# Optimization experiments

Hardware: AMD Instinct MI355X
Metric: run time of the kernel (lower is better)

The kernel has to match this reference:

```python
import jax, jax.numpy as jnp
import numpy as np

N = 50000   # nodes
E = 800000  # edges per timestep
T = 2
IN_C = 128
HID = 128


def gcn_conv(x, src, dst, W, b):
    """PyG GCNConv: add self-loops, symmetric normalization, linear, scatter-add, bias."""
    n = x.shape[0]
    loop = jnp.arange(n, dtype=src.dtype)
    s = jnp.concatenate([src, loop])  # [E+N]
    d = jnp.concatenate([dst, loop])
    h = x @ W                          # [N, H]
    deg = jax.ops.segment_sum(jnp.ones_like(d, dtype=x.dtype), d, num_segments=n)
    dinv = jnp.where(deg > 0, jax.lax.rsqrt(deg), 0.0)
    norm = dinv[s] * dinv[d]           # [E+N]
    msg = h[s] * norm[:, None]         # gather + scale
    out = jax.ops.segment_sum(msg, d, num_segments=n)  # scatter-add
    return out + b


def setup_inputs() -> dict:
    key = jax.random.key(0)
    ks = jax.random.split(key, 6)
    x_seq = jax.random.normal(ks[0], (T, N, IN_C), dtype=jnp.float32)
    edge_indices = jax.random.randint(ks[1], (T, 2, E), 0, N, dtype=jnp.int64)
    W1 = jax.random.normal(ks[2], (IN_C, HID), dtype=jnp.float32) * (1.0 / np.sqrt(IN_C))
    b1 = jnp.zeros((HID,), dtype=jnp.float32)
    W2 = jax.random.normal(ks[3], (HID, HID), dtype=jnp.float32) * (1.0 / np.sqrt(HID))
    b2 = jnp.zeros((HID,), dtype=jnp.float32)
    Wc = jax.random.normal(ks[4], (HID, 1), dtype=jnp.float32) * (1.0 / np.sqrt(HID))
    bc = jnp.zeros((1,), dtype=jnp.float32)
    return {"x_seq": x_seq, "edge_indices": edge_indices, "W1": W1, "b1": b1,
            "W2": W2, "b2": b2, "Wc": Wc, "bc": bc}


def reference(x_seq, edge_indices, W1, b1, W2, b2, Wc, bc):
    outputs = []
    for t in range(T):  # small fixed timestep loop, as in original
        x_t = x_seq[t]
        src = edge_indices[t, 0]
        dst = edge_indices[t, 1]
        h = jax.nn.relu(gcn_conv(x_t, src, dst, W1, b1))
        # dropout is inference-identity (eval mode)
        h = gcn_conv(h, src, dst, W2, b2)
        outputs.append(h)
    final = outputs[-1]
    importance_out = (final @ Wc + bc).squeeze(-1)  # [N]
    return (importance_out, *outputs)
```

## Files before the change

kernel.cpp:

```cpp
#include <hip/hip_runtime.h>
#include <hip/hip_bf16.h>

typedef unsigned int u32;
typedef unsigned short u16;
typedef unsigned long long u64;
typedef __bf16 bf16x8 __attribute__((ext_vector_type(8)));
typedef short short8 __attribute__((ext_vector_type(8)));
typedef float floatx4 __attribute__((ext_vector_type(4)));

__device__ inline float b2f(u16 b) { return __uint_as_float((u32)b << 16); }
__device__ inline float lo2f(u32 p) { return __uint_as_float(p << 16); }
__device__ inline float hi2f(u32 p) { return __uint_as_float(p & 0xffff0000u); }
__device__ inline u16 f2bs(float f) {
    __hip_bfloat16 h = __float2bfloat16(f);
    return *reinterpret_cast<u16*>(&h);
}
__device__ inline float ldext(const void* p, int fl, int i) {
    return fl ? ((const float*)p)[i] : b2f(((const u16*)p)[i]);
}

__global__ __launch_bounds__(64) void detect_kernel(const int* __restrict__ eb,
                                                    const u32* __restrict__ xw,
                                                    int* __restrict__ flags,
                                                    int S, int n) {
    __shared__ int sh[64 * 3];
    int lane = threadIdx.x & 63;
    int zc = 0, explo = 0;
#pragma unroll
    for (int r = 0; r < 4; ++r) {
        int i = 64 * r + lane;
        zc += (eb[2 * i + 1] == 0) ? 1 : 0;
        u32 w = xw[i];
        int e = (int)((w >> 7) & 0xFF);
        explo += (e >= 96 && e <= 140) ? 1 : 0;
    }
    sh[lane] = zc;
    sh[64 + lane] = explo;
    __syncthreads();
    int fl = 0;
    {
        int z = 0;
        for (int j = 0; j < 64; ++j) z += sh[j];
        fl = (z > 200) ? 1 : 0;
    }
    int vc = 0;
#pragma unroll
    for (int r = 0; r < 4; ++r) {
        int li = S / 2 + 64 * r + lane;
        int v = fl ? eb[2 * li] : eb[li];
        vc += ((unsigned)v < (unsigned)n) ? 1 : 0;
    }
    sh[128 + lane] = vc;
    __syncthreads();
    if (lane == 0) {
        int vtot = 0, etot = 0;
        for (int j = 0; j < 64; ++j) vtot += sh[128 + j];
        for (int j = 0; j < 64; ++j) etot += sh[64 + j];
        flags[0] = fl;
        flags[1] = (etot >= 192) ? 0 : 1;
        flags[2] = (vtot >= 240) ? (S / 4) : (S / 8);
    }
}

__device__ inline int load_edge(const int* eb, int fl, int idx) {
    return eb[fl ? (idx << 1) : idx];
}

#define PCHUNK 4096
__global__ __launch_bounds__(256) void part_kernel(const int* __restrict__ eb,
                                                   const int* __restrict__ flags,
                                                   int* __restrict__ bkcnt,
                                                   u64* __restrict__ pairs,
                                                   int n, int shift, int capP) {
    __shared__ int cnt[512];
    __shared__ int gbase[512];
    const int E = flags[2];
    const int fl = flags[0];
    const int nbuk = (2 * n + (1 << shift) - 1) >> shift;
    const int tid = threadIdx.x;
    for (int i = tid; i < nbuk; i += 256) cnt[i] = 0;
    __syncthreads();
    const int e0 = blockIdx.x * PCHUNK;
    int sv[16], gv[16], rk[16];
#pragma unroll
    for (int j = 0; j < 16; ++j) {
        int e = e0 + j * 256 + tid;
        int s = 0, g = -1;
        if (e < 2 * E) {
            int t = (e >= E) ? 1 : 0;
            int le = e - t * E;
            s = load_edge(eb, fl, t * 2 * E + le);
            unsigned du = (unsigned)load_edge(eb, fl, t * 2 * E + E + le);
            if (du < (unsigned)n) g = t * n + (int)du;
        }
        sv[j] = s;
        gv[j] = g;
        rk[j] = (g >= 0) ? atomicAdd(&cnt[g >> shift], 1) : 0;
    }
    __syncthreads();
    for (int b = tid; b < nbuk; b += 256) {
        int c = cnt[b];
        gbase[b] = c ? atomicAdd(&bkcnt[b], c) : 0;
    }
    __syncthreads();
#pragma unroll
    for (int j = 0; j < 16; ++j) {
        if (gv[j] >= 0) {
            int b = gv[j] >> shift;
            int idx = gbase[b] + rk[j];
            if (idx < capP)
                pairs[(size_t)b * capP + idx] =
                    ((u64)(u32)gv[j] << 32) | (u32)sv[j];
        }
    }
}

__global__ __launch_bounds__(256) void scan_bk(const int* __restrict__ bkcnt,
                                               int* __restrict__ bkbase,
                                               int nbuk, int capP) {
    __shared__ int tmp[256];
    int t = threadIdx.x;
    int carry = 0;
    for (int c0 = 0; c0 < nbuk; c0 += 256) {
        int d = 0;
        if (c0 + t < nbuk) {
            d = bkcnt[c0 + t];
            if (d > capP) d = capP;
        }
        int val = d;
        tmp[t] = val;
        __syncthreads();
        for (int o = 1; o < 256; o <<= 1) {
            int add = (t >= o) ? tmp[t - o] : 0;
            __syncthreads();
            val += add;
            tmp[t] = val;
            __syncthreads();
        }
        if (c0 + t < nbuk) bkbase[c0 + t] = val - d + carry;
        int tot = tmp[255];
        __syncthreads();
        carry += tot;
    }
}

__global__ __launch_bounds__(256) void scat_kernel(const u64* __restrict__ pairs,
                                                   const int* __restrict__ bkcnt,
                                                   const int* __restrict__ bkbase,
                                                   int* __restrict__ deg,
                                                   int* __restrict__ off,
                                                   float* __restrict__ dinv,
                                                   int* __restrict__ ssrc,
                                                   int n2, int shift, int capP) {
    __shared__ int hist[1024];
    __shared__ int lscan[256];
    const int b = blockIdx.x;
    const int d0 = b << shift;
    if (d0 >= n2) return;
    int nn = (1 << shift);
    if (d0 + nn > n2) nn = n2 - d0;
    const int tid = threadIdx.x;
    for (int j = tid; j < nn; j += 256) hist[j] = 0;
    __syncthreads();
    int cnt = bkcnt[b];
    if (cnt > capP) cnt = capP;
    const u64* pb = pairs + (size_t)b * capP;
    for (int i = tid; i < cnt; i += 256) {
        unsigned dl = (unsigned)(int)(pb[i] >> 32) - (unsigned)d0;
        if (dl < (unsigned)nn) atomicAdd(&hist[dl], 1);
    }
    __syncthreads();
    int base4 = tid * 4;
    int s0 = 0, s1 = 0, s2 = 0, s3 = 0;
    if (base4 < nn) {
        s0 = hist[base4];
        s1 = (base4 + 1 < nn) ? hist[base4 + 1] : 0;
        s2 = (base4 + 2 < nn) ? hist[base4 + 2] : 0;
        s3 = (base4 + 3 < nn) ? hist[base4 + 3] : 0;
    }
    int tsum = s0 + s1 + s2 + s3;
    lscan[tid] = tsum;
    __syncthreads();
    int val = tsum;
    for (int o = 1; o < 256; o <<= 1) {
        int add = (tid >= o) ? lscan[tid - o] : 0;
        __syncthreads();
        val += add;
        lscan[tid] = val;
        __syncthreads();
    }
    int texcl = val - tsum;
    const int gb = bkbase[b];
    if (base4 < nn) {
        int g = d0 + base4;
        int o0 = gb + texcl;
        deg[g] = s0; off[g] = o0; dinv[g] = rsqrtf((float)(s0 + 1));
        hist[base4] = o0;
        if (base4 + 1 < nn) {
            int o1 = o0 + s0;
            deg[g + 1] = s1; off[g + 1] = o1; dinv[g + 1] = rsqrtf((float)(s1 + 1));
            hist[base4 + 1] = o1;
        }
        if (base4 + 2 < nn) {
            int o2 = o0 + s0 + s1;
            deg[g + 2] = s2; off[g + 2] = o2; dinv[g + 2] = rsqrtf((float)(s2 + 1));
            hist[base4 + 2] = o2;
        }
        if (base4 + 3 < nn) {
            int o3 = o0 + s0 + s1 + s2;
            deg[g + 3] = s3; off[g + 3] = o3; dinv[g + 3] = rsqrtf((float)(s3 + 1));
            hist[base4 + 3] = o3;
        }
    }
    __syncthreads();
    const int limit = gb + cnt;
    for (int i = tid; i < cnt; i += 256) {
        u64 p = pb[i];
        unsigned dl = (unsigned)(int)(p >> 32) - (unsigned)d0;
        if (dl < (unsigned)nn) {
            int pos = atomicAdd(&hist[dl], 1);
            if (pos < limit) ssrc[pos] = (int)(u32)p;
        }
    }
}

__global__ __launch_bounds__(256) void prep_w(const void* __restrict__ W1,
                                              const void* __restrict__ W2,
                                              const int* __restrict__ flags,
                                              u16* __restrict__ W1t,
                                              u16* __restrict__ W2t) {
    int tid = blockIdx.x * 256 + threadIdx.x;
    if (tid < 2 * 128 * 128) {
        int which = tid >> 14;
        int r = tid & 16383;
        const void* W = which ? W2 : W1;
        u16* Wt = which ? W2t : W1t;
        int c = r >> 7, k = r & 127;
        Wt[c * 128 + k] = f2bs(ldext(W, flags[1], k * 128 + c));
    }
}

__global__ __launch_bounds__(256) void gemm_mfma(const void* __restrict__ Xv,
                                                 size_t xoff, int x_ext,
                                                 const u16* __restrict__ Wt,
                                                 const int* __restrict__ flags,
                                                 const float* __restrict__ dinv,
                                                 u16* __restrict__ hs, int n) {
    __shared__ u16 Ws[128 * 136];
    {
        u32* wsu = (u32*)Ws;
        const u32* wtu = (const u32*)Wt;
        for (int i = threadIdx.x; i < 128 * 64; i += 256) {
            int c = i >> 6, kk = i & 63;
            wsu[c * 68 + kk] = wtu[i];
        }
    }
    __syncthreads();

    const int wave = threadIdx.x >> 6;
    const int lane = threadIdx.x & 63;
    const int m = lane & 15;
    const int quad = lane >> 4;
    const int node0 = blockIdx.x * 64 + wave * 16;
    if (node0 >= n) return;

    const int xf32 = x_ext ? flags[1] : 0;
    int va = node0 + m;
    if (va > n - 1) va = n - 1;

    floatx4 acc[8];
#pragma unroll
    for (int t = 0; t < 8; ++t) acc[t] = (floatx4){0.f, 0.f, 0.f, 0.f};

#pragma unroll
    for (int ks = 0; ks < 4; ++ks) {
        bf16x8 a;
        if (xf32) {
            const float* Xf = (const float*)Xv + xoff + (size_t)va * 128 + ks * 32 + quad * 8;
            float4 x0 = *(const float4*)Xf;
            float4 x1 = *(const float4*)(Xf + 4);
            short8 as;
            as[0] = (short)f2bs(x0.x); as[1] = (short)f2bs(x0.y);
            as[2] = (short)f2bs(x0.z); as[3] = (short)f2bs(x0.w);
            as[4] = (short)f2bs(x1.x); as[5] = (short)f2bs(x1.y);
            as[6] = (short)f2bs(x1.z); as[7] = (short)f2bs(x1.w);
            a = __builtin_bit_cast(bf16x8, as);
        } else {
            const u16* Xb = (const u16*)Xv + xoff + (size_t)va * 128 + ks * 32 + quad * 8;
            a = *(const bf16x8*)Xb;
        }
#pragma unroll
        for (int t = 0; t < 8; ++t) {
            const bf16x8 b = *(const bf16x8*)(Ws + (16 * t + m) * 136 + ks * 32 + quad * 8);
            acc[t] = __builtin_amdgcn_mfma_f32_16x16x32_bf16(a, b, acc[t], 0, 0, 0);
        }
    }

#pragma unroll
    for (int r = 0; r < 4; ++r) {
        int v = node0 + quad * 4 + r;
        if (v < n) {
            float dv = dinv[v];
#pragma unroll
            for (int t = 0; t < 8; ++t)
                hs[(size_t)v * 128 + 16 * t + m] = f2bs(acc[t][r] * dv);
        }
    }
}

__global__ __launch_bounds__(256) void gather_kernel(const u16* __restrict__ hs,
                                                     const int* __restrict__ off,
                                                     const int* __restrict__ deg,
                                                     const int* __restrict__ ssrc,
                                                     const float* __restrict__ dinv,
                                                     const void* __restrict__ bias,
                                                     const int* __restrict__ flags,
                                                     float* __restrict__ outf,
                                                     u16* __restrict__ outb,
                                                     const void* __restrict__ Wc,
                                                     const void* __restrict__ bc,
                                                     float* __restrict__ imp,
                                                     int n, int relu) {
    int w = (blockIdx.x * 256 + threadIdx.x) >> 6;
    int lane = threadIdx.x & 63;
    if (w >= n) return;

    const u32* hsu = (const u32*)hs;
    u32 p = hsu[(size_t)w * 64 + lane];
    float ax = lo2f(p), ay = hi2f(p);
    int i = __builtin_amdgcn_readfirstlane(off[w]);
    int end = i + __builtin_amdgcn_readfirstlane(deg[w]);
    unsigned nm1 = (unsigned)(n - 1);

    float bx = 0.f, by = 0.f, cx = 0.f, cy = 0.f, dx = 0.f, dy = 0.f;
    for (; i + 8 <= end; i += 8) {
        unsigned s0 = (unsigned)ssrc[i];     if (s0 > nm1) s0 = 0;
        unsigned s1 = (unsigned)ssrc[i + 1]; if (s1 > nm1) s1 = 0;
        unsigned s2 = (unsigned)ssrc[i + 2]; if (s2 > nm1) s2 = 0;
        unsigned s3 = (unsigned)ssrc[i + 3]; if (s3 > nm1) s3 = 0;
        unsigned s4 = (unsigned)ssrc[i + 4]; if (s4 > nm1) s4 = 0;
        unsigned s5 = (unsigned)ssrc[i + 5]; if (s5 > nm1) s5 = 0;
        unsigned s6 = (unsigned)ssrc[i + 6]; if (s6 > nm1) s6 = 0;
        unsigned s7 = (unsigned)ssrc[i + 7]; if (s7 > nm1) s7 = 0;
        u32 v0 = hsu[(size_t)s0 * 64 + lane];
        u32 v1 = hsu[(size_t)s1 * 64 + lane];
        u32 v2 = hsu[(size_t)s2 * 64 + lane];
        u32 v3 = hsu[(size_t)s3 * 64 + lane];
        u32 v4 = hsu[(size_t)s4 * 64 + lane];
        u32 v5 = hsu[(size_t)s5 * 64 + lane];
        u32 v6 = hsu[(size_t)s6 * 64 + lane];
        u32 v7 = hsu[(size_t)s7 * 64 + lane];
        ax += lo2f(v0); ay += hi2f(v0);
        bx += lo2f(v1); by += hi2f(v1);
        cx += lo2f(v2); cy += hi2f(v2);
        dx += lo2f(v3); dy += hi2f(v3);
        ax += lo2f(v4); ay += hi2f(v4);
        bx += lo2f(v5); by += hi2f(v5);
        cx += lo2f(v6); cy += hi2f(v6);
        dx += lo2f(v7); dy += hi2f(v7);
    }
    for (; i + 4 <= end; i += 4) {
        unsigned s0 = (unsigned)ssrc[i];     if (s0 > nm1) s0 = 0;
        unsigned s1 = (unsigned)ssrc[i + 1]; if (s1 > nm1) s1 = 0;
        unsigned s2 = (unsigned)ssrc[i + 2]; if (s2 > nm1) s2 = 0;
        unsigned s3 = (unsigned)ssrc[i + 3]; if (s3 > nm1) s3 = 0;
        u32 v0 = hsu[(size_t)s0 * 64 + lane];
        u32 v1 = hsu[(size_t)s1 * 64 + lane];
        u32 v2 = hsu[(size_t)s2 * 64 + lane];
        u32 v3 = hsu[(size_t)s3 * 64 + lane];
        ax += lo2f(v0); ay += hi2f(v0);
        bx += lo2f(v1); by += hi2f(v1);
        cx += lo2f(v2); cy += hi2f(v2);
        dx += lo2f(v3); dy += hi2f(v3);
    }
    for (; i < end; ++i) {
        unsigned s = (unsigned)ssrc[i];
        if (s > nm1) s = 0;
        u32 v = hsu[(size_t)s * 64 + lane];
        ax += lo2f(v);
        ay += hi2f(v);
    }
    ax += bx + cx + dx;
    ay += by + cy + dy;

    int ffl = flags[1];
    float dv = dinv[w];
    float o0 = dv * ax + ldext(bias, ffl, 2 * lane);
    float o1 = dv * ay + ldext(bias, ffl, 2 * lane + 1);
    if (relu) {
        o0 = fmaxf(o0, 0.f);
        o1 = fmaxf(o1, 0.f);
    }
    if (outf) ((float2*)outf)[(size_t)w * 64 + lane] = make_float2(o0, o1);
    else ((u32*)outb)[(size_t)w * 64 + lane] = (u32)f2bs(o0) | ((u32)f2bs(o1) << 16);

    if (imp) {
        float cb = o0 * ldext(Wc, ffl, 2 * lane) + o1 * ldext(Wc, ffl, 2 * lane + 1);
        cb += __shfl_xor(cb, 32);
        cb += __shfl_xor(cb, 16);
        cb += __shfl_xor(cb, 8);
        cb += __shfl_xor(cb, 4);
        cb += __shfl_xor(cb, 2);
        cb += __shfl_xor(cb, 1);
        if (lane == 0) imp[w] = cb + ldext(bc, ffl, 0);
    }
}

extern "C" void kernel_launch(void* const* d_in, const int* in_sizes, int n_in,
                              void* d_out, int out_size, void* d_ws, size_t ws_size,
                              hipStream_t stream) {
    const int T = 2, C = 128;
    const int N = in_sizes[0] / (T * C);
    const int S = in_sizes[1];
    const int Emax = S / 4;
    const int N2 = 2 * N;

    const void* x_seq = d_in[0];
    const int* edges = (const int*)d_in[1];
    const void* W1 = d_in[2];
    const void* b1 = d_in[3];
    const void* W2 = d_in[4];
    const void* b2 = d_in[5];
    const void* Wc = d_in[6];
    const void* bc = d_in[7];

    float* out = (float*)d_out;
    float* R0 = out + N;
    float* R1 = out + N + (size_t)N * C;

    char* p = (char*)d_ws;
    auto alloc = [&](size_t bytes) {
        char* r = p;
        p += (bytes + 255) & ~(size_t)255;
        return r;
    };
    int* flags = (int*)alloc(256);
    int* deg = (int*)alloc((size_t)N2 * 4);
    int* off = (int*)alloc((size_t)N2 * 4);
    float* dinv = (float*)alloc((size_t)N2 * 4);
    int* bkcnt = (int*)alloc(512 * 4);
    int* bkbase = (int*)alloc(512 * 4);
    int* ssrc = (int*)alloc((size_t)2 * Emax * 4);
    u16* W1t = (u16*)alloc(128 * 128 * 2);
    u16* W2t = (u16*)alloc(128 * 128 * 2);
    u16* hsb = (u16*)alloc((size_t)N * C * 2);
    u16* hmb = (u16*)alloc((size_t)N * C * 2);
    u64* pairs = (u64*)hsb;

    int shift = 8;
    while ((((N2 + (1 << shift) - 1) >> shift) > 512) && shift < 10) ++shift;
    const int NBUK = (N2 + (1 << shift) - 1) >> shift;
    const size_t aliasBytes = (size_t)2 * N * C * 2;
    int capP = (int)(aliasBytes / (8 * (size_t)NBUK));

    const int gP = (2 * Emax + PCHUNK - 1) / PCHUNK;
    const int gN4 = (N + 3) / 4;
    const int gG = (N + 63) / 64;
    const int gW = (2 * 128 * 128 + 255) / 256;

    detect_kernel<<<1, 64, 0, stream>>>(edges, (const u32*)x_seq, flags, S, N);
    prep_w<<<gW, 256, 0, stream>>>(W1, W2, flags, W1t, W2t);

    hipMemsetAsync(bkcnt, 0, 512 * 4, stream);
    part_kernel<<<gP, 256, 0, stream>>>(edges, flags, bkcnt, pairs, N, shift, capP);
    scan_bk<<<1, 256, 0, stream>>>(bkcnt, bkbase, NBUK, capP);
    scat_kernel<<<NBUK, 256, 0, stream>>>(pairs, bkcnt, bkbase, deg, off, dinv,
                                          ssrc, N2, shift, capP);

    for (int t = 0; t < T; ++t) {
        float* Rt = (t == 0) ? R0 : R1;
        const int* off_t = off + (size_t)t * N;
        const int* deg_t = deg + (size_t)t * N;
        const float* dinv_t = dinv + (size_t)t * N;

        gemm_mfma<<<gG, 256, 0, stream>>>(x_seq, (size_t)t * N * C, 1, W1t, flags,
                                          dinv_t, hsb, N);
        gather_kernel<<<gN4, 256, 0, stream>>>(hsb, off_t, deg_t, ssrc, dinv_t, b1,
                                               flags, (float*)nullptr, hmb,
                                               nullptr, nullptr, (float*)nullptr,
                                               N, 1);

        gemm_mfma<<<gG, 256, 0, stream>>>(hmb, 0, 0, W2t, flags, dinv_t, hsb, N);
        gather_kernel<<<gN4, 256, 0, stream>>>(hsb, off_t, deg_t, ssrc, dinv_t, b2,
                                               flags, Rt, (u16*)nullptr,
                                               Wc, bc, (t == 1) ? out : (float*)nullptr,
                                               N, 0);
    }
}
```

Baseline: 327.8 us.

## Batch both timesteps into single GEMM/gather launches and drop bucket scan

Measured after the change: 293.2 us. 10.5% less time.

```diff
diff --git a/kernel.cpp b/kernel.cpp
--- a/kernel.cpp
+++ b/kernel.cpp
@@ -81,19 +81,19 @@
     for (int i = tid; i < nbuk; i += 256) cnt[i] = 0;
     __syncthreads();
     const int e0 = blockIdx.x * PCHUNK;
-    int sv[16], gv[16], rk[16];
+    u32 sv[16]; int gv[16], rk[16];
 #pragma unroll
     for (int j = 0; j < 16; ++j) {
         int e = e0 + j * 256 + tid;
-        int s = 0, g = -1;
+        u32 gs = 0; int g = -1;
         if (e < 2 * E) {
             int t = (e >= E) ? 1 : 0;
             int le = e - t * E;
-            s = load_edge(eb, fl, t * 2 * E + le);
+            gs = (u32)(t * n) + (u32)load_edge(eb, fl, t * 2 * E + le);
             unsigned du = (unsigned)load_edge(eb, fl, t * 2 * E + E + le);
             if (du < (unsigned)n) g = t * n + (int)du;
         }
-        sv[j] = s;
+        sv[j] = gs;
         gv[j] = g;
         rk[j] = (g >= 0) ? atomicAdd(&cnt[g >> shift], 1) : 0;
     }
@@ -110,43 +110,13 @@
             int idx = gbase[b] + rk[j];
             if (idx < capP)
                 pairs[(size_t)b * capP + idx] =
-                    ((u64)(u32)gv[j] << 32) | (u32)sv[j];
-        }
-    }
-}
-
-__global__ __launch_bounds__(256) void scan_bk(const int* __restrict__ bkcnt,
-                                               int* __restrict__ bkbase,
-                                               int nbuk, int capP) {
-    __shared__ int tmp[256];
-    int t = threadIdx.x;
-    int carry = 0;
-    for (int c0 = 0; c0 < nbuk; c0 += 256) {
-        int d = 0;
-        if (c0 + t < nbuk) {
-            d = bkcnt[c0 + t];
-            if (d > capP) d = capP;
-        }
-        int val = d;
-        tmp[t] = val;
-        __syncthreads();
-        for (int o = 1; o < 256; o <<= 1) {
-            int add = (t >= o) ? tmp[t - o] : 0;
-            __syncthreads();
-            val += add;
-            tmp[t] = val;
-            __syncthreads();
-        }
-        if (c0 + t < nbuk) bkbase[c0 + t] = val - d + carry;
-        int tot = tmp[255];
-        __syncthreads();
-        carry += tot;
+                    ((u64)(u32)gv[j] << 32) | sv[j];
+        }
     }
 }
 
 __global__ __launch_bounds__(256) void scat_kernel(const u64* __restrict__ pairs,
                                                    const int* __restrict__ bkcnt,
-                                                   const int* __restrict__ bkbase,
                                                    int* __restrict__ deg,
                                                    int* __restrict__ off,
                                                    float* __restrict__ dinv,
@@ -164,7 +134,8 @@
     __syncthreads();
     int cnt = bkcnt[b];
     if (cnt > capP) cnt = capP;
-    const u64* pb = pairs + (size_t)b * capP;
+    const int gb = b * capP;
+    const u64* pb = pairs + (size_t)gb;
     for (int i = tid; i < cnt; i += 256) {
         unsigned dl = (unsigned)(int)(pb[i] >> 32) - (unsigned)d0;
         if (dl < (unsigned)nn) atomicAdd(&hist[dl], 1);
@@ -190,7 +161,6 @@
         __syncthreads();
     }
     int texcl = val - tsum;
-    const int gb = bkbase[b];
     if (base4 < nn) {
         int g = d0 + base4;
         int o0 = gb + texcl;
@@ -241,7 +211,7 @@
 }
 
 __global__ __launch_bounds__(256) void gemm_mfma(const void* __restrict__ Xv,
-                                                 size_t xoff, int x_ext,
+                                                 int x_ext,
                                                  const u16* __restrict__ Wt,
                                                  const int* __restrict__ flags,
                                                  const float* __restrict__ dinv,
@@ -276,7 +246,7 @@
     for (int ks = 0; ks < 4; ++ks) {
         bf16x8 a;
         if (xf32) {
-            const float* Xf = (const float*)Xv + xoff + (size_t)va * 128 + ks * 32 + quad * 8;
+            const float* Xf = (const float*)Xv + (size_t)va * 128 + ks * 32 + quad * 8;
             float4 x0 = *(const float4*)Xf;
             float4 x1 = *(const float4*)(Xf + 4);
             short8 as;
@@ -286,7 +256,7 @@
             as[6] = (short)f2bs(x1.z); as[7] = (short)f2bs(x1.w);
             a = __builtin_bit_cast(bf16x8, as);
         } else {
-            const u16* Xb = (const u16*)Xv + xoff + (size_t)va * 128 + ks * 32 + quad * 8;
+            const u16* Xb = (const u16*)Xv + (size_t)va * 128 + ks * 32 + quad * 8;
             a = *(const bf16x8*)Xb;
         }
 #pragma unroll
@@ -320,17 +290,17 @@
                                                      const void* __restrict__ Wc,
                                                      const void* __restrict__ bc,
                                                      float* __restrict__ imp,
-                                                     int n, int relu) {
+                                                     int n2, int half, int relu) {
     int w = (blockIdx.x * 256 + threadIdx.x) >> 6;
     int lane = threadIdx.x & 63;
-    if (w >= n) return;
+    if (w >= n2) return;
 
     const u32* hsu = (const u32*)hs;
     u32 p = hsu[(size_t)w * 64 + lane];
     float ax = lo2f(p), ay = hi2f(p);
     int i = __builtin_amdgcn_readfirstlane(off[w]);
     int end = i + __builtin_amdgcn_readfirstlane(deg[w]);
-    unsigned nm1 = (unsigned)(n - 1);
+    unsigned nm1 = (unsigned)(n2 - 1);
 
     float bx = 0.f, by = 0.f, cx = 0.f, cy = 0.f, dx = 0.f, dy = 0.f;
     for (; i + 8 <= end; i += 8) {
@@ -394,7 +364,7 @@
     if (outf) ((float2*)outf)[(size_t)w * 64 + lane] = make_float2(o0, o1);
     else ((u32*)outb)[(size_t)w * 64 + lane] = (u32)f2bs(o0) | ((u32)f2bs(o1) << 16);
 
-    if (imp) {
+    if (imp && w >= half) {
         float cb = o0 * ldext(Wc, ffl, 2 * lane) + o1 * ldext(Wc, ffl, 2 * lane + 1);
         cb += __shfl_xor(cb, 32);
         cb += __shfl_xor(cb, 16);
@@ -402,7 +372,7 @@
         cb += __shfl_xor(cb, 4);
         cb += __shfl_xor(cb, 2);
         cb += __shfl_xor(cb, 1);
-        if (lane == 0) imp[w] = cb + ldext(bc, ffl, 0);
+        if (lane == 0) imp[w - half] = cb + ldext(bc, ffl, 0);
     }
 }
 
@@ -414,6 +384,7 @@
     const int S = in_sizes[1];
     const int Emax = S / 4;
     const int N2 = 2 * N;
+    (void)Emax;
 
     const void* x_seq = d_in[0];
     const int* edges = (const int*)d_in[1];
@@ -425,8 +396,7 @@
     const void* bc = d_in[7];
 
     float* out = (float*)d_out;
-    float* R0 = out + N;
-    float* R1 = out + N + (size_t)N * C;
+    float* R = out + N;
 
     char* p = (char*)d_ws;
     auto alloc = [&](size_t bytes) {
@@ -439,23 +409,23 @@
     int* off = (int*)alloc((size_t)N2 * 4);
     float* dinv = (float*)alloc((size_t)N2 * 4);
     int* bkcnt = (int*)alloc(512 * 4);
-    int* bkbase = (int*)alloc(512 * 4);
-    int* ssrc = (int*)alloc((size_t)2 * Emax * 4);
-    u16* W1t = (u16*)alloc(128 * 128 * 2);
-    u16* W2t = (u16*)alloc(128 * 128 * 2);
-    u16* hsb = (u16*)alloc((size_t)N * C * 2);
-    u16* hmb = (u16*)alloc((size_t)N * C * 2);
-    u64* pairs = (u64*)hsb;
 
     int shift = 8;
     while ((((N2 + (1 << shift) - 1) >> shift) > 512) && shift < 10) ++shift;
     const int NBUK = (N2 + (1 << shift) - 1) >> shift;
-    const size_t aliasBytes = (size_t)2 * N * C * 2;
-    int capP = (int)(aliasBytes / (8 * (size_t)NBUK));
+    const size_t aliasBytes = (size_t)2 * N2 * C * 2;
+    const int capP = (int)(aliasBytes / (8 * (size_t)NBUK));
+
+    int* ssrc = (int*)alloc((size_t)NBUK * capP * 4);
+    u16* W1t = (u16*)alloc(128 * 128 * 2);
+    u16* W2t = (u16*)alloc(128 * 128 * 2);
+    u16* hsb = (u16*)alloc((size_t)N2 * C * 2);
+    u16* hmb = (u16*)alloc((size_t)N2 * C * 2);
+    u64* pairs = (u64*)hsb;
 
     const int gP = (2 * Emax + PCHUNK - 1) / PCHUNK;
-    const int gN4 = (N + 3) / 4;
-    const int gG = (N + 63) / 64;
+    const int gN2 = (N2 + 3) / 4;
+    const int gG2 = (N2 + 63) / 64;
     const int gW = (2 * 128 * 128 + 255) / 256;
 
     detect_kernel<<<1, 64, 0, stream>>>(edges, (const u32*)x_seq, flags, S, N);
@@ -463,27 +433,18 @@
 
     hipMemsetAsync(bkcnt, 0, 512 * 4, stream);
     part_kernel<<<gP, 256, 0, stream>>>(edges, flags, bkcnt, pairs, N, shift, capP);
-    scan_bk<<<1, 256, 0, stream>>>(bkcnt, bkbase, NBUK, capP);
-    scat_kernel<<<NBUK, 256, 0, stream>>>(pairs, bkcnt, bkbase, deg, off, dinv,
+    scat_kernel<<<NBUK, 256, 0, stream>>>(pairs, bkcnt, deg, off, dinv,
                                           ssrc, N2, shift, capP);
 
-    for (int t = 0; t < T; ++t) {
-        float* Rt = (t == 0) ? R0 : R1;
-        const int* off_t = off + (size_t)t * N;
-        const int* deg_t = deg + (size_t)t * N;
-        const float* dinv_t = dinv + (size_t)t * N;
-
-        gemm_mfma<<<gG, 256, 0, stream>>>(x_seq, (size_t)t * N * C, 1, W1t, flags,
-                                          dinv_t, hsb, N);
-        gather_kernel<<<gN4, 256, 0, stream>>>(hsb, off_t, deg_t, ssrc, dinv_t, b1,
-                                               flags, (float*)nullptr, hmb,
-                                               nullptr, nullptr, (float*)nullptr,
-                                               N, 1);
-
-        gemm_mfma<<<gG, 256, 0, stream>>>(hmb, 0, 0, W2t, flags, dinv_t, hsb, N);
-        gather_kernel<<<gN4, 256, 0, stream>>>(hsb, off_t, deg_t, ssrc, dinv_t, b2,
-                                               flags, Rt, (u16*)nullptr,
-                                               Wc, bc, (t == 1) ? out : (float*)nullptr,
-                                               N, 0);
-    }
-}
+    gemm_mfma<<<gG2, 256, 0, stream>>>(x_seq, 1, W1t, flags, dinv, hsb, N2);
+    gather_kernel<<<gN2, 256, 0, stream>>>(hsb, off, deg, ssrc, dinv, b1, flags,
+                                           (float*)nullptr, hmb,
+                                           nullptr, nullptr, (float*)nullptr,
+                                           N2, N, 1);
+
+    gemm_mfma<<<gG2, 256, 0, stream>>>(hmb, 0, W2t, flags, dinv, hsb, N2);
+    gather_kernel<<<gN2, 256, 0, stream>>>(hsb, off, deg, ssrc, dinv, b2, flags,
+                                           R, (u16*)nullptr,
+                                           Wc, bc, out,
+                                           N2, N, 0);
+}
```
